# Kernel tuning notes

Hardware: AMD Instinct MI355X
Metric: run time of the kernel (lower is better)

Reference implementation:

```python
import jax, jax.numpy as jnp
import numpy as np

E = 256      # embedding_dim
H = 8        # num_heads
D = E // H   # head_dim = 32
F = 1024     # dim_feedforward
EPS = 1e-5


def layer_norm(x, gamma, beta):
    mu = jnp.mean(x, axis=-1, keepdims=True)
    var = jnp.var(x, axis=-1, keepdims=True)
    return (x - mu) * jax.lax.rsqrt(var + EPS) * gamma + beta


def setup_inputs() -> dict:
    key = jax.random.key(0)
    ks = jax.random.split(key, 12)
    s = lambda fan_in: 1.0 / np.sqrt(fan_in)
    src = jax.random.normal(ks[0], (4, 2048, E), dtype=jnp.float32)
    w_in = jax.random.uniform(ks[1], (3 * E, E), minval=-s(E), maxval=s(E), dtype=jnp.float32)
    w_out = jax.random.uniform(ks[2], (E, E), minval=-s(E), maxval=s(E), dtype=jnp.float32)
    w1 = jax.random.uniform(ks[3], (F, E), minval=-s(E), maxval=s(E), dtype=jnp.float32)
    b1 = jax.random.uniform(ks[4], (F,), minval=-s(E), maxval=s(E), dtype=jnp.float32)
    w2 = jax.random.uniform(ks[5], (E, F), minval=-s(F), maxval=s(F), dtype=jnp.float32)
    b2 = jax.random.uniform(ks[6], (E,), minval=-s(F), maxval=s(F), dtype=jnp.float32)
    g1 = jnp.ones((E,), jnp.float32)
    beta1 = jnp.zeros((E,), jnp.float32)
    g2 = jnp.ones((E,), jnp.float32)
    beta2 = jnp.zeros((E,), jnp.float32)
    return {"src": src, "w_in": w_in, "w_out": w_out, "w1": w1, "b1": b1,
            "w2": w2, "b2": b2, "g1": g1, "beta1": beta1, "g2": g2, "beta2": beta2}


def reference(src, w_in, w_out, w1, b1, w2, b2, g1, beta1, g2, beta2):
    B, S, _ = src.shape
    scale = D ** (-0.5)
    # --- pre-norm self-attention block ---
    x = layer_norm(src, g1, beta1)                 # [B,S,E]
    qkv = x @ w_in.T                               # [B,S,3E]
    q, k, v = jnp.split(qkv, 3, axis=-1)
    q = q.reshape(B, S, H, D).transpose(0, 2, 1, 3)  # [B,H,S,D]
    k = k.reshape(B, S, H, D).transpose(0, 2, 1, 3)
    v = v.reshape(B, S, H, D).transpose(0, 2, 1, 3)
    scores = jnp.einsum('bhqd,bhkd->bhqk', q, k) * scale  # [B,H,S,S]
    attn = jax.nn.softmax(scores, axis=-1)
    out = jnp.einsum('bhqk,bhkd->bhqd', attn, v)   # [B,H,S,D]
    out = out.transpose(0, 2, 1, 3).reshape(B, S, E)
    src = src + out @ w_out.T
    # --- pre-norm FFN block ---
    y = layer_norm(src, g2, beta2)
    y = jax.nn.relu(y @ w1.T + b1) @ w2.T + b2
    return src + y
```

## Files before the change

### kernel.cpp

```cpp
#include <hip/hip_runtime.h>
#include <hip/hip_bf16.h>
#include <math.h>

typedef unsigned short u16;
typedef unsigned int   u32;
using bf16x8 = __attribute__((ext_vector_type(8))) short;
using f32x4  = __attribute__((ext_vector_type(4))) float;
using f32x16 = __attribute__((ext_vector_type(16))) float;
using u32v4  = __attribute__((ext_vector_type(4))) u32;

#define TE 256
#define TH 8
#define TS 2048
#define TB 4
#define NTOK 8192
#define QSCALE 0.2550120651552454f
#define EXP2(x) __builtin_amdgcn_exp2f(x)

__device__ __forceinline__ void async16(const u16* g, u16* l) {
    __builtin_amdgcn_global_load_lds(
        (const __attribute__((address_space(1))) u32*)g,
        (__attribute__((address_space(3))) u32*)l, 16, 0, 0);
}
__device__ __forceinline__ u32 pkbf(float a, float b) {
    u32 ua = __float_as_uint(a) + 0x8000u;
    u32 ub = __float_as_uint(b) + 0x8000u;
    return __builtin_amdgcn_perm(ub, ua, 0x07060302u);
}
__device__ __forceinline__ u16 bf1(float a) {
    return (u16)((__float_as_uint(a) + 0x8000u) >> 16);
}

__global__ __launch_bounds__(256) void ln_bf(const float* __restrict__ in,
        u16* __restrict__ out, const float* __restrict__ gamma,
        const float* __restrict__ beta) {
    int row  = blockIdx.x * 4 + (threadIdx.x >> 6);
    int lane = threadIdx.x & 63;
    float4 v = ((const float4*)(in + (size_t)row * TE))[lane];
    float s  = v.x + v.y + v.z + v.w;
    float s2 = v.x*v.x + v.y*v.y + v.z*v.z + v.w*v.w;
    #pragma unroll
    for (int off = 32; off > 0; off >>= 1) {
        s  += __shfl_down(s,  off, 64);
        s2 += __shfl_down(s2, off, 64);
    }
    s  = __shfl(s,  0, 64);
    s2 = __shfl(s2, 0, 64);
    float mu = s * (1.f / TE);
    float rs = rsqrtf(s2 * (1.f / TE) - mu * mu + 1e-5f);
    float4 g = ((const float4*)gamma)[lane];
    float4 b = ((const float4*)beta )[lane];
    u32 lo = pkbf((v.x - mu) * rs * g.x + b.x, (v.y - mu) * rs * g.y + b.y);
    u32 hi = pkbf((v.z - mu) * rs * g.z + b.z, (v.w - mu) * rs * g.w + b.w);
    ((uint2*)(out + (size_t)row * TE))[lane] = make_uint2(lo, hi);
}

__global__ __launch_bounds__(256) void convw(const float* __restrict__ s0, u16* d0,
        const float* __restrict__ s1, u16* d1, const float* __restrict__ s2, u16* d2,
        const float* __restrict__ s3, u16* d3) {
    int i = (blockIdx.x * 256 + threadIdx.x) * 4;
    const float* s; u16* d;
    if      (i < 196608) { s = s0; d = d0; }
    else if (i < 262144) { s = s1; d = d1; i -= 196608; }
    else if (i < 524288) { s = s2; d = d2; i -= 262144; }
    else                 { s = s3; d = d3; i -= 524288; }
    float4 v = *(const float4*)(s + i);
    *(uint2*)(d + i) = make_uint2(pkbf(v.x, v.y), pkbf(v.z, v.w));
}

template<int K, int BM, int EPI>
__global__ __launch_bounds__(256) void mgemm(const u16* __restrict__ A,
        const u16* __restrict__ W, const float* __restrict__ bias,
        const float* __restrict__ R, float* __restrict__ Cf,
        u16* __restrict__ Cb, int M) {
    constexpr int BN = BM;
    __shared__ u16 Al[2][BM * 32];
    __shared__ u16 Wl[2][BN * 32];
    const int tid = threadIdx.x, w = tid >> 6, l = tid & 63;
    const int n0 = blockIdx.y * BM;
    const int m0 = blockIdx.x * BN;
    constexpr int NT = (BM == 128) ? 4 : 2;
    constexpr int NF = (BM == 128) ? 4 : 2;
    const int tw = (w & 1) * NT * 16;
    const int fw = (w >> 1) * NF * 16;
    const int fr = l & 15, fq = l >> 4;
    const int sr = l >> 2, sc = (l & 3) * 8;
    f32x4 acc[NT][NF];
    #pragma unroll
    for (int t = 0; t < NT; t++)
        #pragma unroll
        for (int f = 0; f < NF; f++)
            #pragma unroll
            for (int r = 0; r < 4; r++) acc[t][f][r] = 0.f;

    for (int k0 = 0; k0 < K; k0 += 64) {
        __syncthreads();
        #pragma unroll
        for (int hh = 0; hh < 2; hh++) {
            const int kc = k0 + hh * 32;
            if (BM == 128) {
                #pragma unroll
                for (int c = 0; c < 2; c++) {
                    int rr = (w * 2 + c) * 16 + sr;
                    async16(A + (size_t)(n0 + rr) * K + kc + sc, &Al[hh][(w * 2 + c) * 512]);
                    async16(W + (size_t)(m0 + rr) * K + kc + sc, &Wl[hh][(w * 2 + c) * 512]);
                }
            } else {
                int rr = w * 16 + sr;
                async16(A + (size_t)(n0 + rr) * K + kc + sc, &Al[hh][w * 512]);
                async16(W + (size_t)(m0 + rr) * K + kc + sc, &Wl[hh][w * 512]);
            }
        }
        __syncthreads();
        #pragma unroll
        for (int hh = 0; hh < 2; hh++) {
            bf16x8 af[NT], wf[NF];
            #pragma unroll
            for (int t = 0; t < NT; t++)
                af[t] = *(const bf16x8*)&Al[hh][(tw + t * 16 + fr) * 32 + fq * 8];
            #pragma unroll
            for (int f = 0; f < NF; f++)
                wf[f] = *(const bf16x8*)&Wl[hh][(fw + f * 16 + fr) * 32 + fq * 8];
            #pragma unroll
            for (int t = 0; t < NT; t++)
                #pragma unroll
                for (int f = 0; f < NF; f++)
                    acc[t][f] = __builtin_amdgcn_mfma_f32_16x16x32_bf16(
                        wf[f], af[t], acc[t][f], 0, 0, 0);
        }
    }
    #pragma unroll
    for (int t = 0; t < NT; t++) {
        const int tok = n0 + tw + t * 16 + fr;
        #pragma unroll
        for (int f = 0; f < NF; f++) {
            const int fb = m0 + fw + f * 16 + fq * 4;
            f32x4 v = acc[t][f];
            if (EPI == 0) {
                if (fb < 256) {
                    *(uint2*)(Cb + (size_t)tok * 256 + fb) = make_uint2(
                        pkbf(v[0]*QSCALE, v[1]*QSCALE), pkbf(v[2]*QSCALE, v[3]*QSCALE));
                } else if (fb < 512) {
                    const int hh = (fb - 256) >> 5, dd = (fb - 256) & 31;
                    const int bh = (tok >> 11) * 8 + hh;
                    const int kv = tok & 2047, tile = kv >> 5, lq = kv & 31;
                    const int fg = dd >> 4, hg = (dd >> 3) & 1, j = dd & 7;
                    u16* kp = (u16*)bias +
                        (((((size_t)bh * 64 + tile) * 2 + fg) * 2 + hg) * 32 + lq) * 8 + j;
                    *(uint2*)kp = make_uint2(pkbf(v[0], v[1]), pkbf(v[2], v[3]));
                } else {
                    const int hh = (fb - 512) >> 5, dd = (fb - 512) & 31;
                    const int bh = (tok >> 11) * 8 + hh;
                    const int kv = tok & 2047, tile = kv >> 5, kvr = kv & 31;
                    const int fg = kvr >> 4, hg = (kvr >> 3) & 1, j = kvr & 7;
                    u16* vp = (u16*)R +
                        ((((size_t)bh * 64 + tile) * 2 + fg) * 2 + hg) * 256 +
                        (size_t)dd * 8 + j;
                    vp[0]  = bf1(v[0]);
                    vp[8]  = bf1(v[1]);
                    vp[16] = bf1(v[2]);
                    vp[24] = bf1(v[3]);
                }
            } else if (EPI == 1) {
                float4 r4 = *(const float4*)(R + (size_t)tok * M + fb);
                *(float4*)(Cf + (size_t)tok * M + fb) =
                    make_float4(v[0]+r4.x, v[1]+r4.y, v[2]+r4.z, v[3]+r4.w);
            } else if (EPI == 2) {
                float4 b4 = *(const float4*)(bias + fb);
                *(uint2*)(Cb + (size_t)tok * M + fb) = make_uint2(
                    pkbf(fmaxf(v[0]+b4.x, 0.f), fmaxf(v[1]+b4.y, 0.f)),
                    pkbf(fmaxf(v[2]+b4.z, 0.f), fmaxf(v[3]+b4.w, 0.f)));
            } else {
                float4 b4 = *(const float4*)(bias + fb);
                float4 r4 = *(const float4*)(R + (size_t)tok * M + fb);
                *(float4*)(Cf + (size_t)tok * M + fb) = make_float4(
                    v[0]+b4.x+r4.x, v[1]+b4.y+r4.y, v[2]+b4.z+r4.z, v[3]+b4.w+r4.w);
            }
        }
    }
}

__global__ __launch_bounds__(256, 4) void attn_k(const u16* __restrict__ qb,
        const u16* __restrict__ kfb, const u16* __restrict__ vfb,
        u16* __restrict__ attn) {
    const int id = blockIdx.x;
    const int bh   = (id & 7) * 4 + (id >> 8);
    const int tile = (id >> 3) & 31;
    const int b = bh >> 3, h = bh & 7;
    const int tid = threadIdx.x, w = tid >> 6, l = tid & 63;
    const int qw = w & 1, kw = w >> 1;
    const int lq = l & 31, hi = l >> 5;
    const size_t btok = (size_t)b * TS;
    const int q0 = tile * 64 + qw * 32;

    __shared__ float mrg[2304];

    const u16* qrow = qb + (btok + q0 + lq) * 256 + h * 32 + hi * 8;
    bf16x8 qf0 = *(const bf16x8*)qrow;
    bf16x8 qf1 = *(const bf16x8*)(qrow + 16);

    f32x16 zf, o;
    #pragma unroll
    for (int r = 0; r < 16; r++) { zf[r] = 0.f; o[r] = 0.f; }
    float ps = 0.f;

    const u16* kp = kfb + ((size_t)bh * 64 + kw * 32) * 1024 + l * 8;
    const u16* vp = vfb + ((size_t)bh * 64 + kw * 32) * 1024 + l * 8;
    bf16x8 k0 = *(const bf16x8*)kp;
    bf16x8 k1 = *(const bf16x8*)(kp + 512);
    bf16x8 v0 = *(const bf16x8*)vp;
    bf16x8 v1 = *(const bf16x8*)(vp + 512);

    #pragma unroll 2
    for (int it = 0; it < 32; ++it) {
        kp += 1024; vp += 1024;
        bf16x8 nk0 = *(const bf16x8*)kp;
        bf16x8 nk1 = *(const bf16x8*)(kp + 512);
        bf16x8 nv0 = *(const bf16x8*)vp;
        bf16x8 nv1 = *(const bf16x8*)(vp + 512);
        f32x16 p = __builtin_amdgcn_mfma_f32_32x32x16_bf16(k0, qf0, zf, 0, 0, 0);
        p = __builtin_amdgcn_mfma_f32_32x32x16_bf16(k1, qf1, p, 0, 0, 0);
        float e[16];
        #pragma unroll
        for (int r = 0; r < 16; r++) e[r] = EXP2(p[r]);
        ps += ((e[0]+e[1]) + (e[2]+e[3])) + ((e[4]+e[5]) + (e[6]+e[7]))
            + ((e[8]+e[9]) + (e[10]+e[11])) + ((e[12]+e[13]) + (e[14]+e[15]));
        u32 a[8];
        #pragma unroll
        for (int j = 0; j < 8; j++)
            asm("v_cvt_pk_bf16_f32 %0, %1, %2"
                : "=v"(a[j]) : "v"(e[2*j]), "v"(e[2*j+1]));
        asm("v_permlane32_swap_b32 %0, %1" : "+v"(a[0]), "+v"(a[2]));
        asm("v_permlane32_swap_b32 %0, %1" : "+v"(a[1]), "+v"(a[3]));
        asm("v_permlane32_swap_b32 %0, %1" : "+v"(a[4]), "+v"(a[6]));
        asm("v_permlane32_swap_b32 %0, %1" : "+v"(a[5]), "+v"(a[7]));
        u32v4 t0 = {a[0], a[1], a[2], a[3]};
        u32v4 t1 = {a[4], a[5], a[6], a[7]};
        bf16x8 pf0 = __builtin_bit_cast(bf16x8, t0);
        bf16x8 pf1 = __builtin_bit_cast(bf16x8, t1);
        o = __builtin_amdgcn_mfma_f32_32x32x16_bf16(v0, pf0, o, 0, 0, 0);
        o = __builtin_amdgcn_mfma_f32_32x32x16_bf16(v1, pf1, o, 0, 0, 0);
        k0 = nk0; k1 = nk1; v0 = nv0; v1 = nv1;
    }
    ps += __shfl_xor(ps, 32, 64);

    if (kw == 1) {
        float* d = mrg + (qw * 64 + l) * 18;
        #pragma unroll
        for (int r = 0; r < 16; r++) d[r] = o[r];
        d[16] = ps;
    }
    __syncthreads();
    if (kw == 0) {
        const float* d = mrg + (qw * 64 + l) * 18;
        #pragma unroll
        for (int r = 0; r < 16; r++) o[r] += d[r];
        ps += d[16];
        float inv = 1.f / ps;
        int tok = (int)btok + q0 + lq;
        u16* orow = attn + (size_t)tok * 256 + h * 32 + hi * 4;
        #pragma unroll
        for (int g = 0; g < 4; g++)
            *(uint2*)(orow + g * 8) = make_uint2(
                pkbf(o[4*g]*inv, o[4*g+1]*inv), pkbf(o[4*g+2]*inv, o[4*g+3]*inv));
    }
}

extern "C" void kernel_launch(void* const* d_in, const int* in_sizes, int n_in,
                              void* d_out, int out_size, void* d_ws, size_t ws_size,
                              hipStream_t stream) {
    const float* src  = (const float*)d_in[0];
    const float* w_in = (const float*)d_in[1];
    const float* w_out= (const float*)d_in[2];
    const float* w1   = (const float*)d_in[3];
    const float* b1   = (const float*)d_in[4];
    const float* w2   = (const float*)d_in[5];
    const float* b2   = (const float*)d_in[6];
    const float* g1   = (const float*)d_in[7];
    const float* be1  = (const float*)d_in[8];
    const float* g2   = (const float*)d_in[9];
    const float* be2  = (const float*)d_in[10];
    float* out = (float*)d_out;

    u16* xb    = (u16*)d_ws;
    u16* qb    = xb + (size_t)NTOK * 256;
    u16* kfbuf = qb + (size_t)NTOK * 256;
    u16* vfbuf = kfbuf + (size_t)32 * 64 * 1024;
    u16* attnb = xb;
    u16* h1b   = (u16*)d_ws;
    u16* x2b   = (u16*)((char*)d_ws + (size_t)NTOK * 1024 * 2);
    u16* wib   = x2b + (size_t)NTOK * 256;
    u16* wob   = wib + 768 * 256;
    u16* w1b   = wob + 256 * 256;
    u16* w2b   = w1b + 1024 * 256;

    convw<<<768, 256, 0, stream>>>(w_in, wib, w_out, wob, w1, w1b, w2, w2b);
    ln_bf<<<NTOK / 4, 256, 0, stream>>>(src, xb, g1, be1);
    mgemm<256, 128, 0><<<dim3(6, 64), 256, 0, stream>>>(
        xb, wib, (const float*)kfbuf, (const float*)vfbuf, nullptr, qb, 768);
    attn_k<<<dim3(1024), 256, 0, stream>>>(qb, kfbuf, vfbuf, attnb);
    mgemm<256, 64, 1><<<dim3(4, 128), 256, 0, stream>>>(
        attnb, wob, nullptr, src, out, nullptr, 256);
    ln_bf<<<NTOK / 4, 256, 0, stream>>>(out, x2b, g2, be2);
    mgemm<256, 128, 2><<<dim3(8, 64), 256, 0, stream>>>(
        x2b, w1b, b1, nullptr, nullptr, h1b, 1024);
    mgemm<1024, 64, 3><<<dim3(4, 128), 256, 0, stream>>>(
        h1b, w2b, b2, out, out, nullptr, 256);
}
```

Before: 160.9 us.

## Double-buffer GEMM k-loop with prefetch and fuse weight conversion with first layernorm

The GEMM main loop now issues the async global-to-LDS loads for the next 32-wide k slice before computing on the current buffer. That leaves one barrier per slice instead of a load/barrier/compute/barrier sequence, so memory latency can overlap the MFMA work. Separately, the fp32-to-bf16 weight conversion and the first layernorm are merged into a single launch that dispatches on block index, removing one kernel launch. The cost is a larger barrier count per unit of K, since each barrier now covers a 32-wide slice instead of 64, and correctness depends on the barrier also waiting for the async LDS loads.

```diff
diff --git a/kernel.cpp b/kernel.cpp
--- a/kernel.cpp
+++ b/kernel.cpp
@@ -31,10 +31,10 @@
     return (u16)((__float_as_uint(a) + 0x8000u) >> 16);
 }
 
-__global__ __launch_bounds__(256) void ln_bf(const float* __restrict__ in,
+__device__ __forceinline__ void ln_body(const float* __restrict__ in,
         u16* __restrict__ out, const float* __restrict__ gamma,
-        const float* __restrict__ beta) {
-    int row  = blockIdx.x * 4 + (threadIdx.x >> 6);
+        const float* __restrict__ beta, int rowblk) {
+    int row  = rowblk * 4 + (threadIdx.x >> 6);
     int lane = threadIdx.x & 63;
     float4 v = ((const float4*)(in + (size_t)row * TE))[lane];
     float s  = v.x + v.y + v.z + v.w;
@@ -55,17 +55,29 @@
     ((uint2*)(out + (size_t)row * TE))[lane] = make_uint2(lo, hi);
 }
 
-__global__ __launch_bounds__(256) void convw(const float* __restrict__ s0, u16* d0,
+__global__ __launch_bounds__(256) void ln_bf(const float* __restrict__ in,
+        u16* __restrict__ out, const float* __restrict__ gamma,
+        const float* __restrict__ beta) {
+    ln_body(in, out, gamma, beta, blockIdx.x);
+}
+
+__global__ __launch_bounds__(256) void prep(const float* __restrict__ s0, u16* d0,
         const float* __restrict__ s1, u16* d1, const float* __restrict__ s2, u16* d2,
-        const float* __restrict__ s3, u16* d3) {
-    int i = (blockIdx.x * 256 + threadIdx.x) * 4;
-    const float* s; u16* d;
-    if      (i < 196608) { s = s0; d = d0; }
-    else if (i < 262144) { s = s1; d = d1; i -= 196608; }
-    else if (i < 524288) { s = s2; d = d2; i -= 262144; }
-    else                 { s = s3; d = d3; i -= 524288; }
-    float4 v = *(const float4*)(s + i);
-    *(uint2*)(d + i) = make_uint2(pkbf(v.x, v.y), pkbf(v.z, v.w));
+        const float* __restrict__ s3, u16* d3, const float* __restrict__ src,
+        u16* __restrict__ xb, const float* __restrict__ g1,
+        const float* __restrict__ be1) {
+    if (blockIdx.x < 768) {
+        int i = (blockIdx.x * 256 + threadIdx.x) * 4;
+        const float* s; u16* d;
+        if      (i < 196608) { s = s0; d = d0; }
+        else if (i < 262144) { s = s1; d = d1; i -= 196608; }
+        else if (i < 524288) { s = s2; d = d2; i -= 262144; }
+        else                 { s = s3; d = d3; i -= 524288; }
+        float4 v = *(const float4*)(s + i);
+        *(uint2*)(d + i) = make_uint2(pkbf(v.x, v.y), pkbf(v.z, v.w));
+    } else {
+        ln_body(src, xb, g1, be1, blockIdx.x - 768);
+    }
 }
 
 template<int K, int BM, int EPI>
@@ -74,6 +86,7 @@
         const float* __restrict__ R, float* __restrict__ Cf,
         u16* __restrict__ Cb, int M) {
     constexpr int BN = BM;
+    constexpr int NS = K / 32;
     __shared__ u16 Al[2][BM * 32];
     __shared__ u16 Wl[2][BN * 32];
     const int tid = threadIdx.x, w = tid >> 6, l = tid & 63;
@@ -93,41 +106,42 @@
             #pragma unroll
             for (int r = 0; r < 4; r++) acc[t][f][r] = 0.f;
 
-    for (int k0 = 0; k0 < K; k0 += 64) {
-        __syncthreads();
-        #pragma unroll
-        for (int hh = 0; hh < 2; hh++) {
-            const int kc = k0 + hh * 32;
-            if (BM == 128) {
-                #pragma unroll
-                for (int c = 0; c < 2; c++) {
-                    int rr = (w * 2 + c) * 16 + sr;
-                    async16(A + (size_t)(n0 + rr) * K + kc + sc, &Al[hh][(w * 2 + c) * 512]);
-                    async16(W + (size_t)(m0 + rr) * K + kc + sc, &Wl[hh][(w * 2 + c) * 512]);
-                }
-            } else {
-                int rr = w * 16 + sr;
-                async16(A + (size_t)(n0 + rr) * K + kc + sc, &Al[hh][w * 512]);
-                async16(W + (size_t)(m0 + rr) * K + kc + sc, &Wl[hh][w * 512]);
+    auto stage = [&](int s, int buf) {
+        const int kc = s * 32;
+        if constexpr (BM == 128) {
+            #pragma unroll
+            for (int c = 0; c < 2; c++) {
+                const int rr = (w * 2 + c) * 16 + sr;
+                async16(A + (size_t)(n0 + rr) * K + kc + sc, &Al[buf][(w * 2 + c) * 512]);
+                async16(W + (size_t)(m0 + rr) * K + kc + sc, &Wl[buf][(w * 2 + c) * 512]);
             }
+        } else {
+            const int rr = w * 16 + sr;
+            async16(A + (size_t)(n0 + rr) * K + kc + sc, &Al[buf][w * 512]);
+            async16(W + (size_t)(m0 + rr) * K + kc + sc, &Wl[buf][w * 512]);
         }
-        __syncthreads();
-        #pragma unroll
-        for (int hh = 0; hh < 2; hh++) {
-            bf16x8 af[NT], wf[NF];
-            #pragma unroll
-            for (int t = 0; t < NT; t++)
-                af[t] = *(const bf16x8*)&Al[hh][(tw + t * 16 + fr) * 32 + fq * 8];
+    };
+
+    stage(0, 0);
+    __syncthreads();
+    #pragma unroll 2
+    for (int s = 0; s < NS; ++s) {
+        const int buf = s & 1;
+        if (s + 1 < NS) stage(s + 1, buf ^ 1);
+        bf16x8 af[NT], wf[NF];
+        #pragma unroll
+        for (int t = 0; t < NT; t++)
+            af[t] = *(const bf16x8*)&Al[buf][(tw + t * 16 + fr) * 32 + fq * 8];
+        #pragma unroll
+        for (int f = 0; f < NF; f++)
+            wf[f] = *(const bf16x8*)&Wl[buf][(fw + f * 16 + fr) * 32 + fq * 8];
+        #pragma unroll
+        for (int t = 0; t < NT; t++)
             #pragma unroll
             for (int f = 0; f < NF; f++)
-                wf[f] = *(const bf16x8*)&Wl[hh][(fw + f * 16 + fr) * 32 + fq * 8];
-            #pragma unroll
-            for (int t = 0; t < NT; t++)
-                #pragma unroll
-                for (int f = 0; f < NF; f++)
-                    acc[t][f] = __builtin_amdgcn_mfma_f32_16x16x32_bf16(
-                        wf[f], af[t], acc[t][f], 0, 0, 0);
-        }
+                acc[t][f] = __builtin_amdgcn_mfma_f32_16x16x32_bf16(
+                    wf[f], af[t], acc[t][f], 0, 0, 0);
+        __syncthreads();
     }
     #pragma unroll
     for (int t = 0; t < NT; t++) {
@@ -294,8 +308,8 @@
     u16* w1b   = wob + 256 * 256;
     u16* w2b   = w1b + 1024 * 256;
 
-    convw<<<768, 256, 0, stream>>>(w_in, wib, w_out, wob, w1, w1b, w2, w2b);
-    ln_bf<<<NTOK / 4, 256, 0, stream>>>(src, xb, g1, be1);
+    prep<<<768 + NTOK / 4, 256, 0, stream>>>(
+        w_in, wib, w_out, wob, w1, w1b, w2, w2b, src, xb, g1, be1);
     mgemm<256, 128, 0><<<dim3(6, 64), 256, 0, stream>>>(
         xb, wib, (const float*)kfbuf, (const float*)vfbuf, nullptr, qb, 768);
     attn_k<<<dim3(1024), 256, 0, stream>>>(qb, kfbuf, vfbuf, attnb);
```

New measurement: 166.4 us. +3.4%, slower.
